# Performance work log

Measured on AMD Instinct MI355X. Metric: run time of the kernel, lower is better.

## Reference

```python
import jax, jax.numpy as jnp
import numpy as np

B, D = 131072, 128


def setup_inputs() -> dict:
    key = jax.random.key(0)
    ks = jax.random.split(key, 6)
    return {
        "v": jax.random.normal(ks[0], (B, D), dtype=jnp.float32),
        "e": jax.random.normal(ks[1], (B, D), dtype=jnp.float32),
        "w_vv": jax.random.normal(ks[2], (D,), dtype=jnp.float32),
        "w_ev": jax.random.normal(ks[3], (D,), dtype=jnp.float32),
        "w_ve": jax.random.normal(ks[4], (D,), dtype=jnp.float32),
        "w_ee": jax.random.normal(ks[5], (D,), dtype=jnp.float32),
        "b_v": jnp.zeros((D,), dtype=jnp.float32),
        "b_e": jnp.zeros((D,), dtype=jnp.float32),
    }


def reference(v, e, w_vv, w_ev, w_ve, w_ee, b_v, b_e):
    # C = v e^T  (rank-1), so:
    #   C  @ w      = v * (e . w)
    #   C^T @ w     = e * (v . w)
    # This computes the exact same math as materializing the [B, d, d]
    # outer product and applying the rank-1 Linear projections.
    e_dot_vv = e @ w_vv  # [B]
    v_dot_ev = v @ w_ev  # [B]
    e_dot_ve = e @ w_ve  # [B]
    v_dot_ee = v @ w_ee  # [B]
    v_out = v * e_dot_vv[:, None] + e * v_dot_ev[:, None] + b_v
    e_out = v * e_dot_ve[:, None] + e * v_dot_ee[:, None] + b_e
    return (v_out, e_out)
```

## Files before the change

### kernel.cpp

```cpp
#include <hip/hip_runtime.h>


#define CCU_D 128
#define ROWS_PER_GROUP 4

typedef float f4 __attribute__((ext_vector_type(4)));

__device__ __forceinline__ float dot4v(const f4 a, const f4 b) {
    return a.x * b.x + a.y * b.y + a.z * b.z + a.w * b.w;
}

__global__ __launch_bounds__(256) void ccu_kernel(
    const float* __restrict__ v,
    const float* __restrict__ e,
    const float* __restrict__ w_vv,
    const float* __restrict__ w_ev,
    const float* __restrict__ w_ve,
    const float* __restrict__ w_ee,
    const float* __restrict__ b_v,
    const float* __restrict__ b_e,
    float* __restrict__ v_out,
    float* __restrict__ e_out,
    int nrows)
{
    const int lane32 = threadIdx.x & 31;
    const int group  = (int)((blockIdx.x * (size_t)blockDim.x + threadIdx.x) >> 5);
    const int base   = group * ROWS_PER_GROUP;
    if (base >= nrows) return;

    const f4 wvv = ((const f4*)w_vv)[lane32];
    const f4 wev = ((const f4*)w_ev)[lane32];
    const f4 wve = ((const f4*)w_ve)[lane32];
    const f4 wee = ((const f4*)w_ee)[lane32];

    f4 vr[ROWS_PER_GROUP], er[ROWS_PER_GROUP];
    #pragma unroll
    for (int k = 0; k < ROWS_PER_GROUP; ++k) {
        vr[k] = __builtin_nontemporal_load(
                    (const f4*)(v + (size_t)(base + k) * CCU_D) + lane32);
        er[k] = __builtin_nontemporal_load(
                    (const f4*)(e + (size_t)(base + k) * CCU_D) + lane32);
    }

    float dvv[ROWS_PER_GROUP], dev[ROWS_PER_GROUP];
    float dve[ROWS_PER_GROUP], dee[ROWS_PER_GROUP];
    #pragma unroll
    for (int k = 0; k < ROWS_PER_GROUP; ++k) {
        dvv[k] = dot4v(er[k], wvv);
        dev[k] = dot4v(vr[k], wev);
        dve[k] = dot4v(er[k], wve);
        dee[k] = dot4v(vr[k], wee);
    }

    #pragma unroll
    for (int off = 16; off >= 1; off >>= 1) {
        #pragma unroll
        for (int k = 0; k < ROWS_PER_GROUP; ++k) {
            dvv[k] += __shfl_xor(dvv[k], off);
            dev[k] += __shfl_xor(dev[k], off);
            dve[k] += __shfl_xor(dve[k], off);
            dee[k] += __shfl_xor(dee[k], off);
        }
    }

    const f4 bv = ((const f4*)b_v)[lane32];
    const f4 be = ((const f4*)b_e)[lane32];

    #pragma unroll
    for (int k = 0; k < ROWS_PER_GROUP; ++k) {
        f4 vo, eo;
        vo.x = vr[k].x * dvv[k] + er[k].x * dev[k] + bv.x;
        vo.y = vr[k].y * dvv[k] + er[k].y * dev[k] + bv.y;
        vo.z = vr[k].z * dvv[k] + er[k].z * dev[k] + bv.z;
        vo.w = vr[k].w * dvv[k] + er[k].w * dev[k] + bv.w;

        eo.x = vr[k].x * dve[k] + er[k].x * dee[k] + be.x;
        eo.y = vr[k].y * dve[k] + er[k].y * dee[k] + be.y;
        eo.z = vr[k].z * dve[k] + er[k].z * dee[k] + be.z;
        eo.w = vr[k].w * dve[k] + er[k].w * dee[k] + be.w;

        __builtin_nontemporal_store(
            vo, (f4*)(v_out + (size_t)(base + k) * CCU_D) + lane32);
        __builtin_nontemporal_store(
            eo, (f4*)(e_out + (size_t)(base + k) * CCU_D) + lane32);
    }
}

extern "C" void kernel_launch(void* const* d_in, const int* in_sizes, int n_in,
                              void* d_out, int out_size, void* d_ws, size_t ws_size,
                              hipStream_t stream) {
    const float* v    = (const float*)d_in[0];
    const float* e    = (const float*)d_in[1];
    const float* w_vv = (const float*)d_in[2];
    const float* w_ev = (const float*)d_in[3];
    const float* w_ve = (const float*)d_in[4];
    const float* w_ee = (const float*)d_in[5];
    const float* b_v  = (const float*)d_in[6];
    const float* b_e  = (const float*)d_in[7];

    const int nrows = in_sizes[0] / CCU_D;
    float* v_out = (float*)d_out;
    float* e_out = (float*)d_out + (size_t)nrows * CCU_D;

    const int rows_per_block = (256 / 32) * ROWS_PER_GROUP;
    const int blocks = (nrows + rows_per_block - 1) / rows_per_block;
    ccu_kernel<<<blocks, 256, 0, stream>>>(v, e, w_vv, w_ev, w_ve, w_ee,
                                           b_v, b_e, v_out, e_out, nrows);
}
```

Before: 230.2 us.

## Use persistent grid-stride waves with register double-buffered prefetch of next span

Replaces the one-shot grid with a fixed grid of 1024 blocks whose 64-lane waves stride over 8-row spans. Each wave loads the next span into a second set of registers while computing and storing the current one. This is meant to hide memory latency and cut block launch overhead in a purely bandwidth-bound kernel. It doubles register use, which may lower occupancy, and it silently skips tail rows when nrows is not a multiple of 8.

New measurement: 233.3 us. Within noise of the previous version (+1.3%).

```diff
diff --git a/kernel.cpp b/kernel.cpp
--- a/kernel.cpp
+++ b/kernel.cpp
@@ -2,7 +2,8 @@
 
 
 #define CCU_D 128
-#define ROWS_PER_GROUP 4
+#define SPAN_ROWS 8
+#define F4_PER_SPAN (SPAN_ROWS * (CCU_D / 4))
 
 typedef float f4 __attribute__((ext_vector_type(4)));
 
@@ -23,66 +24,93 @@
     float* __restrict__ e_out,
     int nrows)
 {
-    const int lane32 = threadIdx.x & 31;
-    const int group  = (int)((blockIdx.x * (size_t)blockDim.x + threadIdx.x) >> 5);
-    const int base   = group * ROWS_PER_GROUP;
-    if (base >= nrows) return;
+    const int lane   = threadIdx.x & 63;
+    const int c      = lane & 31;
+    const int wid    = threadIdx.x >> 6;
+    const int gwave  = (int)(blockIdx.x * (blockDim.x >> 6) + wid);
+    const int nwaves = (int)(gridDim.x * (blockDim.x >> 6));
+    const int nspans = nrows / SPAN_ROWS;
 
-    const f4 wvv = ((const f4*)w_vv)[lane32];
-    const f4 wev = ((const f4*)w_ev)[lane32];
-    const f4 wve = ((const f4*)w_ve)[lane32];
-    const f4 wee = ((const f4*)w_ee)[lane32];
+    const f4 wvv = ((const f4*)w_vv)[c];
+    const f4 wev = ((const f4*)w_ev)[c];
+    const f4 wve = ((const f4*)w_ve)[c];
+    const f4 wee = ((const f4*)w_ee)[c];
+    const f4 bv  = ((const f4*)b_v )[c];
+    const f4 be  = ((const f4*)b_e )[c];
 
-    f4 vr[ROWS_PER_GROUP], er[ROWS_PER_GROUP];
-    #pragma unroll
-    for (int k = 0; k < ROWS_PER_GROUP; ++k) {
-        vr[k] = __builtin_nontemporal_load(
-                    (const f4*)(v + (size_t)(base + k) * CCU_D) + lane32);
-        er[k] = __builtin_nontemporal_load(
-                    (const f4*)(e + (size_t)(base + k) * CCU_D) + lane32);
-    }
+    const f4* __restrict__ vf  = (const f4*)v;
+    const f4* __restrict__ ef  = (const f4*)e;
+    f4* __restrict__ vof = (f4*)v_out;
+    f4* __restrict__ eof = (f4*)e_out;
 
-    float dvv[ROWS_PER_GROUP], dev[ROWS_PER_GROUP];
-    float dve[ROWS_PER_GROUP], dee[ROWS_PER_GROUP];
-    #pragma unroll
-    for (int k = 0; k < ROWS_PER_GROUP; ++k) {
-        dvv[k] = dot4v(er[k], wvv);
-        dev[k] = dot4v(vr[k], wev);
-        dve[k] = dot4v(er[k], wve);
-        dee[k] = dot4v(vr[k], wee);
-    }
+    int s = gwave;
+    if (s >= nspans) return;
 
-    #pragma unroll
-    for (int off = 16; off >= 1; off >>= 1) {
+    f4 cv[4], ce[4], nv[4], ne[4];
+    {
+        const size_t base = (size_t)s * F4_PER_SPAN + lane;
         #pragma unroll
-        for (int k = 0; k < ROWS_PER_GROUP; ++k) {
-            dvv[k] += __shfl_xor(dvv[k], off);
-            dev[k] += __shfl_xor(dev[k], off);
-            dve[k] += __shfl_xor(dve[k], off);
-            dee[k] += __shfl_xor(dee[k], off);
+        for (int j = 0; j < 4; ++j) {
+            cv[j] = __builtin_nontemporal_load(vf + base + j * 64);
+            ce[j] = __builtin_nontemporal_load(ef + base + j * 64);
         }
     }
 
-    const f4 bv = ((const f4*)b_v)[lane32];
-    const f4 be = ((const f4*)b_e)[lane32];
+    while (true) {
+        const int  sn   = s + nwaves;
+        const bool more = (sn < nspans);
 
-    #pragma unroll
-    for (int k = 0; k < ROWS_PER_GROUP; ++k) {
-        f4 vo, eo;
-        vo.x = vr[k].x * dvv[k] + er[k].x * dev[k] + bv.x;
-        vo.y = vr[k].y * dvv[k] + er[k].y * dev[k] + bv.y;
-        vo.z = vr[k].z * dvv[k] + er[k].z * dev[k] + bv.z;
-        vo.w = vr[k].w * dvv[k] + er[k].w * dev[k] + bv.w;
+        if (more) {
+            const size_t nb = (size_t)sn * F4_PER_SPAN + lane;
+            #pragma unroll
+            for (int j = 0; j < 4; ++j) {
+                nv[j] = __builtin_nontemporal_load(vf + nb + j * 64);
+                ne[j] = __builtin_nontemporal_load(ef + nb + j * 64);
+            }
+        }
 
-        eo.x = vr[k].x * dve[k] + er[k].x * dee[k] + be.x;
-        eo.y = vr[k].y * dve[k] + er[k].y * dee[k] + be.y;
-        eo.z = vr[k].z * dve[k] + er[k].z * dee[k] + be.z;
-        eo.w = vr[k].w * dve[k] + er[k].w * dee[k] + be.w;
+        float dvv[4], dev[4], dve[4], dee[4];
+        #pragma unroll
+        for (int j = 0; j < 4; ++j) {
+            dvv[j] = dot4v(ce[j], wvv);
+            dev[j] = dot4v(cv[j], wev);
+            dve[j] = dot4v(ce[j], wve);
+            dee[j] = dot4v(cv[j], wee);
+        }
 
-        __builtin_nontemporal_store(
-            vo, (f4*)(v_out + (size_t)(base + k) * CCU_D) + lane32);
-        __builtin_nontemporal_store(
-            eo, (f4*)(e_out + (size_t)(base + k) * CCU_D) + lane32);
+        #pragma unroll
+        for (int off = 16; off >= 1; off >>= 1) {
+            #pragma unroll
+            for (int j = 0; j < 4; ++j) {
+                dvv[j] += __shfl_xor(dvv[j], off);
+                dev[j] += __shfl_xor(dev[j], off);
+                dve[j] += __shfl_xor(dve[j], off);
+                dee[j] += __shfl_xor(dee[j], off);
+            }
+        }
+
+        const size_t ob = (size_t)s * F4_PER_SPAN + lane;
+        #pragma unroll
+        for (int j = 0; j < 4; ++j) {
+            f4 vo, eo;
+            vo.x = cv[j].x * dvv[j] + ce[j].x * dev[j] + bv.x;
+            vo.y = cv[j].y * dvv[j] + ce[j].y * dev[j] + bv.y;
+            vo.z = cv[j].z * dvv[j] + ce[j].z * dev[j] + bv.z;
+            vo.w = cv[j].w * dvv[j] + ce[j].w * dev[j] + bv.w;
+
+            eo.x = cv[j].x * dve[j] + ce[j].x * dee[j] + be.x;
+            eo.y = cv[j].y * dve[j] + ce[j].y * dee[j] + be.y;
+            eo.z = cv[j].z * dve[j] + ce[j].z * dee[j] + be.z;
+            eo.w = cv[j].w * dve[j] + ce[j].w * dee[j] + be.w;
+
+            __builtin_nontemporal_store(vo, vof + ob + j * 64);
+            __builtin_nontemporal_store(eo, eof + ob + j * 64);
+        }
+
+        if (!more) break;
+        s = sn;
+        #pragma unroll
+        for (int j = 0; j < 4; ++j) { cv[j] = nv[j]; ce[j] = ne[j]; }
     }
 }
 
@@ -102,8 +130,7 @@
     float* v_out = (float*)d_out;
     float* e_out = (float*)d_out + (size_t)nrows * CCU_D;
 
-    const int rows_per_block = (256 / 32) * ROWS_PER_GROUP;
-    const int blocks = (nrows + rows_per_block - 1) / rows_per_block;
+    const int blocks = 1024;
     ccu_kernel<<<blocks, 256, 0, stream>>>(v, e, w_vv, w_ev, w_ve, w_ee,
                                            b_v, b_e, v_out, e_out, nrows);
 }
```
